# Performance work log

Measured on AMD Instinct MI355X. Metric: run time of the kernel, lower is better.

The kernel has to match this reference:

```python
import jax, jax.numpy as jnp
import numpy as np

GROUPS = 32
EPS = 1e-5

def group_norm(x, scale, bias):
    b, c, h, w = x.shape
    xg = x.reshape(b, GROUPS, c // GROUPS, h, w)
    mean = xg.mean(axis=(2, 3, 4), keepdims=True)
    var = xg.var(axis=(2, 3, 4), keepdims=True)
    xg = (xg - mean) * jax.lax.rsqrt(var + EPS)
    x = xg.reshape(b, c, h, w)
    return x * scale[None, :, None, None] + bias[None, :, None, None]

def conv2d(x, w, b, pad):
    y = jax.lax.conv_general_dilated(
        x, w, window_strides=(1, 1), padding=[(pad, pad), (pad, pad)],
        dimension_numbers=('NCHW', 'OIHW', 'NCHW'))
    return y + b[None, :, None, None]

def setup_inputs() -> dict:
    key = jax.random.key(0)
    ks = jax.random.split(key, 16)
    B, Cin, Cout, H, W, TDIM, NCON = 4, 128, 128, 64, 64, 512, 4
    s = 0.05
    return {
        'x': jax.random.normal(ks[0], (B, Cin, H, W), jnp.float32),
        't': jax.random.normal(ks[1], (B, TDIM), jnp.float32),
        'aim': jax.random.randint(ks[2], (B,), 0, NCON),
        'cond': jax.random.normal(ks[3], (B, Cin, H, W), jnp.float32),
        'gn1_scale': jnp.ones((Cin,), jnp.float32),
        'gn1_bias': jnp.zeros((Cin,), jnp.float32),
        'conv1_w': jax.random.normal(ks[4], (Cout, Cin, 3, 3), jnp.float32) * s,
        'conv1_b': jnp.zeros((Cout,), jnp.float32),
        'mlp_w': jax.random.normal(ks[5], (Cout, TDIM), jnp.float32) * s,
        'mlp_b': jnp.zeros((Cout,), jnp.float32),
        'cond_w': jax.random.normal(ks[6], (Cout, Cin, 1, 1), jnp.float32) * s,
        'cond_b': jnp.zeros((Cout,), jnp.float32),
        'gn2_scale': jnp.ones((Cout,), jnp.float32),
        'gn2_bias': jnp.zeros((Cout,), jnp.float32),
        'conv2_w': jax.random.normal(ks[7], (Cout, Cout, 3, 3), jnp.float32) * s,
        'conv2_b': jnp.zeros((Cout,), jnp.float32),
        'contrast_embed': jax.random.normal(ks[8], (NCON, Cout, 1, 1), jnp.float32),
    }

def reference(x, t, aim, cond, gn1_scale, gn1_bias, conv1_w, conv1_b,
              mlp_w, mlp_b, cond_w, cond_b, gn2_scale, gn2_bias,
              conv2_w, conv2_b, contrast_embed):
    # block1: GN -> SiLU -> 3x3 conv
    h = conv2d(jax.nn.silu(group_norm(x, gn1_scale, gn1_bias)), conv1_w, conv1_b, 1)
    # time embedding: SiLU -> Linear, broadcast over spatial
    temb = jax.nn.silu(t) @ mlp_w.T + mlp_b  # (b, out_ch)
    h = h + temb[:, :, None, None]
    # spatial cross-attention with cond
    c = conv2d(cond, cond_w, cond_b, 0)  # 1x1 projection, (b, C, u, v)
    C = h.shape[1]
    score = jnp.einsum('bchw,bcuv->bhwuv', h, c)  # (b, h, w, u, v)
    # NOTE: softmax over dim=1 (the spatial h axis), as in the source
    score = jax.nn.softmax(score / jnp.sqrt(jnp.float32(C)), axis=1)
    h = h + jnp.einsum('bhwuv,bcuv->bchw', score, c)
    # contrast embedding lookup
    h = h + contrast_embed[aim]  # (b, C, 1, 1) broadcast
    # block2: GN -> SiLU -> (dropout=identity at eval) -> 3x3 conv
    h = conv2d(jax.nn.silu(group_norm(h, gn2_scale, gn2_bias)), conv2_w, conv2_b, 1)
    # res_conv is Identity since in_ch == out_ch
    return h + x
```

## Files before the change

### kernel.cpp

```cpp
#include <hip/hip_runtime.h>
#include <cmath>

#define BB 4
#define CC 128
#define HH 64
#define WW 64
#define SP 4096
#define NG 32
#define TT 64
#define NS 2
#define PSZ ((size_t)BB * SP * CC)

typedef __bf16 bf16x8 __attribute__((ext_vector_type(8)));
typedef __bf16 bf16x4 __attribute__((ext_vector_type(4)));
typedef float  f32x4  __attribute__((ext_vector_type(4)));

__device__ __forceinline__ float silu_f(float v) {
    return v / (1.f + __expf(-v));
}

__global__ __launch_bounds__(256) void prep_kernel(
    const float* __restrict__ x, const float* __restrict__ gn1s,
    const float* __restrict__ gn1b, __bf16* __restrict__ aT,
    const float* __restrict__ c1w, const float* __restrict__ c2w,
    __bf16* __restrict__ wt,
    const float* __restrict__ t, const float* __restrict__ mlpw,
    const float* __restrict__ mlpb, float* __restrict__ tembw,
    const float* __restrict__ cond, const float* __restrict__ cw,
    const float* __restrict__ cb, __bf16* __restrict__ cmT,
    __bf16* __restrict__ cm2)
{
    __shared__ __align__(16) char pool[18432];
    __shared__ float rs[4], rs2[4], mean_s, inv_s;
    const int blk = blockIdx.x;
    const int tid = threadIdx.x;

    if (blk < 128) {
        const int b = blk >> 5, g = blk & 31;
        const float* p = x + (size_t)blk * 16384;
        float s = 0.f, s2 = 0.f;
        for (int it = 0; it < 16; ++it) {
            int q = it * 256 + tid;
            float4 v = *(const float4*)&p[q * 4];
            s += v.x + v.y + v.z + v.w;
            s2 += v.x * v.x + v.y * v.y + v.z * v.z + v.w * v.w;
        }
        #pragma unroll
        for (int off = 32; off >= 1; off >>= 1) {
            s  += __shfl_down(s,  off, 64);
            s2 += __shfl_down(s2, off, 64);
        }
        const int wid = tid >> 6;
        if ((tid & 63) == 0) { rs[wid] = s; rs2[wid] = s2; }
        __syncthreads();
        if (tid == 0) {
            float S = rs[0] + rs[1] + rs[2] + rs[3];
            float S2 = rs2[0] + rs2[1] + rs2[2] + rs2[3];
            float m = S * (1.f / 16384.f);
            float var = S2 * (1.f / 16384.f) - m * m;
            mean_s = m;
            inv_s = rsqrtf(var + 1e-5f);
        }
        __syncthreads();
        const float m = mean_s, inv = inv_s;
        float sc[4], bi[4];
        #pragma unroll
        for (int j = 0; j < 4; ++j) { sc[j] = gn1s[g * 4 + j]; bi[j] = gn1b[g * 4 + j]; }
        for (int it = 0; it < 16; ++it) {
            int pp = it * 256 + tid;
            bf16x4 o;
            #pragma unroll
            for (int j = 0; j < 4; ++j)
                o[j] = (__bf16)silu_f((p[j * 4096 + pp] - m) * inv * sc[j] + bi[j]);
            *(bf16x4*)&aT[((size_t)(b * SP + pp)) * CC + g * 4] = o;
        }
    } else if (blk < 146) {
        const int idx = blk - 128;
        const int wsel = idx / 9, tap = idx % 9;
        const float* src = wsel ? c2w : c1w;
        __bf16* dst = wt + (size_t)wsel * 9 * 16384 + (size_t)tap * 16384;
        for (int it = 0; it < 64; ++it) {
            int q = it * 256 + tid;
            dst[q] = (__bf16)src[(size_t)q * 9 + tap];
        }
    } else if (blk < 154) {
        const int cog = blk - 146;
        float* st = (float*)pool;
        for (int it = 0; it < 8; ++it) {
            int q = it * 256 + tid;
            st[q] = silu_f(t[q]);
        }
        __syncthreads();
        const int col = tid >> 4, seg = tid & 15;
        const float* wr = mlpw + (size_t)(cog * 16 + col) * 512 + seg * 32;
        float acc[4] = {0.f, 0.f, 0.f, 0.f};
        #pragma unroll
        for (int k8 = 0; k8 < 8; ++k8) {
            float4 wv = *(const float4*)&wr[k8 * 4];
            #pragma unroll
            for (int j = 0; j < 4; ++j) {
                int k = seg * 32 + k8 * 4 + j;
                float w4 = (&wv.x)[j];
                acc[0] += st[0 * 512 + k] * w4;
                acc[1] += st[1 * 512 + k] * w4;
                acc[2] += st[2 * 512 + k] * w4;
                acc[3] += st[3 * 512 + k] * w4;
            }
        }
        #pragma unroll
        for (int o = 1; o < 16; o <<= 1) {
            #pragma unroll
            for (int b4 = 0; b4 < 4; ++b4)
                acc[b4] += __shfl_xor(acc[b4], o, 64);
        }
        if (seg == 0) {
            float bv = mlpb[cog * 16 + col];
            #pragma unroll
            for (int b4 = 0; b4 < 4; ++b4)
                tembw[b4 * 128 + cog * 16 + col] = acc[b4] + bv;
        }
    } else {
        const int pblk = blk - 154;
        const int b = pblk >> 6;
        const int p0 = (pblk & 63) * 64;
        const int l = tid & 63, wv = tid >> 6;
        const int l15 = l & 15, l4 = l >> 4;
        const int mB = wv * 32;

        __bf16* XT = (__bf16*)pool;

        for (int it = 0; it < 32; ++it) {
            int q = it * 256 + tid;
            float v = cond[((size_t)(b * CC + (q >> 6))) * SP + p0 + (q & 63)];
            XT[(q & 63) * 136 + (q >> 6)] = (__bf16)v;
        }
        __syncthreads();

        f32x4 acc[2][4];
        #pragma unroll
        for (int mb = 0; mb < 2; ++mb)
            #pragma unroll
            for (int nt = 0; nt < 4; ++nt) acc[mb][nt] = (f32x4){0.f, 0.f, 0.f, 0.f};

        #pragma unroll
        for (int ks = 0; ks < 4; ++ks) {
            bf16x8 bfr[4];
            #pragma unroll
            for (int nt = 0; nt < 4; ++nt)
                bfr[nt] = *(const bf16x8*)&XT[(nt * 16 + l15) * 136 + ks * 32 + l4 * 8];
            #pragma unroll
            for (int mb = 0; mb < 2; ++mb) {
                const float* wrow = cw + (size_t)(mB + mb * 16 + l15) * 128 + ks * 32 + l4 * 8;
                float4 wa = *(const float4*)wrow;
                float4 wb4 = *(const float4*)(wrow + 4);
                bf16x8 afr;
                afr[0] = (__bf16)wa.x; afr[1] = (__bf16)wa.y;
                afr[2] = (__bf16)wa.z; afr[3] = (__bf16)wa.w;
                afr[4] = (__bf16)wb4.x; afr[5] = (__bf16)wb4.y;
                afr[6] = (__bf16)wb4.z; afr[7] = (__bf16)wb4.w;
                #pragma unroll
                for (int nt = 0; nt < 4; ++nt)
                    acc[mb][nt] = __builtin_amdgcn_mfma_f32_16x16x32_bf16(afr, bfr[nt], acc[mb][nt], 0, 0, 0);
            }
        }

        const float scl = 0.088388347648318447f;
        #pragma unroll
        for (int mb = 0; mb < 2; ++mb) {
            int co0 = mB + mb * 16 + l4 * 4;
            float bv[4];
            #pragma unroll
            for (int r = 0; r < 4; ++r) bv[r] = cb[co0 + r];
            #pragma unroll
            for (int nt = 0; nt < 4; ++nt) {
                int p = p0 + nt * 16 + l15;
                bf16x4 o;
                #pragma unroll
                for (int r = 0; r < 4; ++r)
                    o[r] = (__bf16)((acc[mb][nt][r] + bv[r]) * scl);
                *(bf16x4*)&cmT[((size_t)(b * SP + p)) * CC + co0] = o;
            }
        }
        __syncthreads();
        __bf16* O2 = (__bf16*)pool;
        #pragma unroll
        for (int mb = 0; mb < 2; ++mb) {
            int co0 = mB + mb * 16 + l4 * 4;
            #pragma unroll
            for (int r = 0; r < 4; ++r) {
                float bv = cb[co0 + r];
                #pragma unroll
                for (int nt = 0; nt < 4; ++nt)
                    O2[(co0 + r) * 72 + nt * 16 + l15] = (__bf16)(acc[mb][nt][r] + bv);
            }
        }
        __syncthreads();
        #pragma unroll
        for (int it = 0; it < 4; ++it) {
            int q = it * 256 + tid;
            int co = q >> 3, pc = q & 7;
            *(bf16x8*)&cm2[((size_t)(b * CC + co)) * SP + p0 + pc * 8] =
                *(const bf16x8*)&O2[co * 72 + pc * 8];
        }
    }
}

template<bool FUSE_TEMB, bool OUT_CF>
__global__ __launch_bounds__(256, 4) void conv_mfma_kernel(
    const __bf16* __restrict__ inT, const __bf16* __restrict__ wt,
    const float* __restrict__ bias, const float* __restrict__ temb,
    const float* __restrict__ resid, __bf16* __restrict__ outT,
    float* __restrict__ outF)
{
    const int y   = blockIdx.x >> 2;
    const int xh2 = (blockIdx.x >> 1) & 1;
    const int coh = blockIdx.x & 1;
    const int x0  = xh2 * 32;
    const int b   = blockIdx.y;
    const int tid = threadIdx.x;
    const int l = tid & 63, wv = tid >> 6;
    const int l15 = l & 15, l4 = l >> 4;
    const int co_w = coh * 64 + wv * 16;

    __shared__ __bf16 inS[3 * 16 * 34 * 8];

    const __bf16* inTb = inT + (size_t)b * SP * CC;
    for (int q = tid; q < 3 * 34 * 16; q += 256) {
        int cc = q & 15;
        int t2 = q >> 4;
        int xs = t2 % 34;
        int r  = t2 / 34;
        int yy = y + r - 1;
        int xg = x0 + xs - 1;
        bf16x8 v;
        if (((unsigned)yy < 64u) && ((unsigned)xg < 64u)) {
            v = *(const bf16x8*)&inTb[((size_t)(yy * 64 + xg)) * CC + cc * 8];
        } else {
            #pragma unroll
            for (int j = 0; j < 8; ++j) v[j] = (__bf16)0.f;
        }
        *(bf16x8*)&inS[((r * 16 + cc) * 34 + xs) * 8] = v;
    }
    __syncthreads();

    f32x4 acc[2];
    acc[0] = (f32x4){0.f, 0.f, 0.f, 0.f};
    acc[1] = (f32x4){0.f, 0.f, 0.f, 0.f};

    const __bf16* wp = wt + (size_t)(co_w + l15) * 128 + l4 * 8;
    bf16x8 wb[2][4];
    #pragma unroll
    for (int ks = 0; ks < 4; ++ks)
        wb[0][ks] = *(const bf16x8*)(wp + ks * 32);

    #pragma unroll
    for (int tap = 0; tap < 9; ++tap) {
        const int cur = tap & 1, nxt = cur ^ 1;
        if (tap < 8) {
            #pragma unroll
            for (int ks = 0; ks < 4; ++ks)
                wb[nxt][ks] = *(const bf16x8*)(wp + (tap + 1) * 16384 + ks * 32);
        }
        const int rr = tap / 3, dx = tap % 3;
        #pragma unroll
        for (int ks = 0; ks < 4; ++ks) {
            const __bf16* rb = &inS[((rr * 16 + ks * 4 + l4) * 34) * 8];
            bf16x8 b0 = *(const bf16x8*)&rb[(dx + l15) * 8];
            bf16x8 b1 = *(const bf16x8*)&rb[(16 + dx + l15) * 8];
            acc[0] = __builtin_amdgcn_mfma_f32_16x16x32_bf16(wb[cur][ks], b0, acc[0], 0, 0, 0);
            acc[1] = __builtin_amdgcn_mfma_f32_16x16x32_bf16(wb[cur][ks], b1, acc[1], 0, 0, 0);
        }
    }

    if (OUT_CF) {
        #pragma unroll
        for (int r = 0; r < 4; ++r) {
            int co = co_w + l4 * 4 + r;
            float bv = bias[co];
            #pragma unroll
            for (int nb = 0; nb < 2; ++nb) {
                int p = y * 64 + x0 + nb * 16 + l15;
                size_t o = ((size_t)(b * CC + co)) * SP + p;
                outF[o] = acc[nb][r] + bv + resid[o];
            }
        }
    } else {
        int co0 = co_w + l4 * 4;
        float bv[4];
        #pragma unroll
        for (int r = 0; r < 4; ++r)
            bv[r] = bias[co0 + r] + (FUSE_TEMB ? temb[b * CC + co0 + r] : 0.f);
        #pragma unroll
        for (int nb = 0; nb < 2; ++nb) {
            int p = y * 64 + x0 + nb * 16 + l15;
            bf16x4 o;
            #pragma unroll
            for (int r = 0; r < 4; ++r)
                o[r] = (__bf16)(acc[nb][r] + bv[r]);
            *(bf16x4*)&outT[((size_t)(b * SP + p)) * CC + co0] = o;
        }
    }
}

#define CT2 72
#define PBS 72
#define POOL_BYTES 46080

__global__ __launch_bounds__(256, 3) void attn_kernel(
    const __bf16* __restrict__ h1T, const __bf16* __restrict__ cmT,
    const __bf16* __restrict__ cm2, __bf16* __restrict__ parts)
{
    const int w = blockIdx.x;
    const int b = blockIdx.y;
    const int s = blockIdx.z;
    const int tid = threadIdx.x;
    const int wl = tid >> 6;
    const int l = tid & 63, l15 = l & 15, l4 = l >> 4;
    const int hB = (wl & 1) * 32;
    const int cB = (wl >> 1) * 64;

    __shared__ __align__(16) char pool[POOL_BYTES];
    __bf16* ct2p = (__bf16*)pool;
    __bf16* Pb   = (__bf16*)(pool + 36864);
    __bf16* Otr  = (__bf16*)pool;

    const __bf16* h1Tb = h1T + (size_t)b * SP * CC;
    const __bf16* cmTb = cmT + (size_t)b * SP * CC;
    const __bf16* cm2b = cm2 + (size_t)b * CC * SP;

    bf16x8 hfr[4][4];
    #pragma unroll
    for (int nt = 0; nt < 4; ++nt)
        #pragma unroll
        for (int ks = 0; ks < 4; ++ks)
            hfr[nt][ks] = *(const bf16x8*)&h1Tb[((size_t)((nt * 16 + l15) * WW + w)) * CC + ks * 32 + l4 * 8];

    f32x4 acc2[2][4];
    #pragma unroll
    for (int mb = 0; mb < 2; ++mb)
        #pragma unroll
        for (int nt = 0; nt < 4; ++nt) acc2[mb][nt] = (f32x4){0.f, 0.f, 0.f, 0.f};

    const int sc = tid >> 3;
    const int stc = tid & 7;

    {
        const int uv0 = s * TT;
        #pragma unroll
        for (int it = 0; it < 4; ++it) {
            int c = it * 32 + sc;
            *(bf16x8*)&ct2p[c * CT2 + stc * 8] =
                *(const bf16x8*)&cm2b[(size_t)c * SP + uv0 + stc * 8];
        }
        const __bf16* arow = cmTb + (size_t)(uv0 + 16 * wl + l15) * CC;
        bf16x8 afr[4];
        #pragma unroll
        for (int ks = 0; ks < 4; ++ks) afr[ks] = *(const bf16x8*)&arow[ks * 32 + l4 * 8];
        f32x4 s1[4];
        #pragma unroll
        for (int nt = 0; nt < 4; ++nt) {
            s1[nt] = (f32x4){0.f, 0.f, 0.f, 0.f};
            #pragma unroll
            for (int ks = 0; ks < 4; ++ks)
                s1[nt] = __builtin_amdgcn_mfma_f32_16x16x32_bf16(afr[ks], hfr[nt][ks], s1[nt], 0, 0, 0);
        }
        #pragma unroll
        for (int r = 0; r < 4; ++r) {
            float e0 = __expf(s1[0][r]), e1 = __expf(s1[1][r]);
            float e2 = __expf(s1[2][r]), e3 = __expf(s1[3][r]);
            float sm = e0 + e1 + e2 + e3;
            sm += __shfl_xor(sm, 1, 64);
            sm += __shfl_xor(sm, 2, 64);
            sm += __shfl_xor(sm, 4, 64);
            sm += __shfl_xor(sm, 8, 64);
            float ri = 1.f / sm;
            s1[0][r] = e0 * ri; s1[1][r] = e1 * ri;
            s1[2][r] = e2 * ri; s1[3][r] = e3 * ri;
        }
        #pragma unroll
        for (int nt = 0; nt < 4; ++nt) {
            bf16x4 pk;
            pk[0] = (__bf16)s1[nt][0]; pk[1] = (__bf16)s1[nt][1];
            pk[2] = (__bf16)s1[nt][2]; pk[3] = (__bf16)s1[nt][3];
            *(bf16x4*)&Pb[(nt * 16 + l15) * PBS + 16 * wl + l4 * 4] = pk;
        }
    }

    for (int i = 0; i < SP / TT / NS; ++i) {
        const int cur = i & 1;
        __syncthreads();
        bf16x8 st4[4];
        bf16x8 afr[4];
        if (i < SP / TT / NS - 1) {
            const int uv0n = ((i + 1) * NS + s) * TT;
            #pragma unroll
            for (int it = 0; it < 4; ++it) {
                int c = it * 32 + sc;
                st4[it] = *(const bf16x8*)&cm2b[(size_t)c * SP + uv0n + stc * 8];
            }
            const __bf16* arow = cmTb + (size_t)(uv0n + 16 * wl + l15) * CC;
            #pragma unroll
            for (int ks = 0; ks < 4; ++ks) afr[ks] = *(const bf16x8*)&arow[ks * 32 + l4 * 8];
        }
        bf16x8 pfr[2][2];
        #pragma unroll
        for (int mb = 0; mb < 2; ++mb)
            #pragma unroll
            for (int ks = 0; ks < 2; ++ks)
                pfr[mb][ks] = *(const bf16x8*)&Pb[(hB + mb * 16 + l15) * PBS + ks * 32 + l4 * 8];
        __syncthreads();
        {
            const __bf16* ctR = ct2p + cur * 9216;
            #pragma unroll
            for (int mb = 0; mb < 2; ++mb)
                #pragma unroll
                for (int nt = 0; nt < 4; ++nt)
                    #pragma unroll
                    for (int ks = 0; ks < 2; ++ks) {
                        bf16x8 bfr = *(const bf16x8*)&ctR[(cB + nt * 16 + l15) * CT2 + ks * 32 + l4 * 8];
                        acc2[mb][nt] = __builtin_amdgcn_mfma_f32_16x16x32_bf16(
                            pfr[mb][ks], bfr, acc2[mb][nt], 0, 0, 0);
                    }
        }
        if (i < SP / TT / NS - 1) {
            __bf16* ctW = ct2p + (cur ^ 1) * 9216;
            #pragma unroll
            for (int it = 0; it < 4; ++it) {
                int c = it * 32 + sc;
                *(bf16x8*)&ctW[c * CT2 + stc * 8] = st4[it];
            }
            f32x4 s1[4];
            #pragma unroll
            for (int nt = 0; nt < 4; ++nt) {
                s1[nt] = (f32x4){0.f, 0.f, 0.f, 0.f};
                #pragma unroll
                for (int ks = 0; ks < 4; ++ks)
                    s1[nt] = __builtin_amdgcn_mfma_f32_16x16x32_bf16(afr[ks], hfr[nt][ks], s1[nt], 0, 0, 0);
            }
            #pragma unroll
            for (int r = 0; r < 4; ++r) {
                float e0 = __expf(s1[0][r]), e1 = __expf(s1[1][r]);
                float e2 = __expf(s1[2][r]), e3 = __expf(s1[3][r]);
                float sm = e0 + e1 + e2 + e3;
                sm += __shfl_xor(sm, 1, 64);
                sm += __shfl_xor(sm, 2, 64);
                sm += __shfl_xor(sm, 4, 64);
                sm += __shfl_xor(sm, 8, 64);
                float ri = 1.f / sm;
                s1[0][r] = e0 * ri; s1[1][r] = e1 * ri;
                s1[2][r] = e2 * ri; s1[3][r] = e3 * ri;
            }
            #pragma unroll
            for (int nt = 0; nt < 4; ++nt) {
                bf16x4 pk;
                pk[0] = (__bf16)s1[nt][0]; pk[1] = (__bf16)s1[nt][1];
                pk[2] = (__bf16)s1[nt][2]; pk[3] = (__bf16)s1[nt][3];
                *(bf16x4*)&Pb[(nt * 16 + l15) * PBS + 16 * wl + l4 * 4] = pk;
            }
        }
    }

    __syncthreads();
    #pragma unroll
    for (int mb = 0; mb < 2; ++mb)
        #pragma unroll
        for (int nt = 0; nt < 4; ++nt)
            #pragma unroll
            for (int r = 0; r < 4; ++r)
                Otr[(hB + mb * 16 + l4 * 4 + r) * 136 + cB + nt * 16 + l15] =
                    (__bf16)acc2[mb][nt][r];
    __syncthreads();
    __bf16* pO = parts + (size_t)s * PSZ;
    #pragma unroll
    for (int it = 0; it < 4; ++it) {
        int q = it * 256 + tid;
        int h = q >> 4, cc = q & 15;
        *(bf16x8*)&pO[((size_t)(b * SP + h * WW + w)) * CC + cc * 8] =
            *(const bf16x8*)&Otr[h * 136 + cc * 8];
    }
}

__global__ __launch_bounds__(256) void gn2_stats_kernel(
    const __bf16* __restrict__ h1T, const __bf16* __restrict__ parts,
    const int* __restrict__ aim, const float* __restrict__ emb,
    __bf16* __restrict__ h2T, float* __restrict__ pstat)
{
    const int pb = blockIdx.x, b = blockIdx.y;
    const int tid = threadIdx.x;
    const int c4 = tid & 31;
    const float4 ev = *(const float4*)&emb[aim[b] * CC + c4 * 4];
    float s = 0.f, s2 = 0.f;
    for (int it = 0; it < 8; ++it) {
        int prow = it * 8 + (tid >> 5);
        size_t base = ((size_t)(b * SP + pb * 64 + prow)) * CC + c4 * 4;
        bf16x4 hv = *(const bf16x4*)&h1T[base];
        float v0 = (float)hv[0] + ev.x;
        float v1 = (float)hv[1] + ev.y;
        float v2 = (float)hv[2] + ev.z;
        float v3 = (float)hv[3] + ev.w;
        #pragma unroll
        for (int k = 0; k < NS; ++k) {
            bf16x4 a = *(const bf16x4*)&parts[(size_t)k * PSZ + base];
            v0 += (float)a[0]; v1 += (float)a[1];
            v2 += (float)a[2]; v3 += (float)a[3];
        }
        bf16x4 o;
        o[0] = (__bf16)v0; o[1] = (__bf16)v1;
        o[2] = (__bf16)v2; o[3] = (__bf16)v3;
        *(bf16x4*)&h2T[base] = o;
        s += v0 + v1 + v2 + v3;
        s2 += v0 * v0 + v1 * v1 + v2 * v2 + v3 * v3;
    }
    s  += __shfl_down(s,  32, 64);
    s2 += __shfl_down(s2, 32, 64);
    __shared__ float ls[4][32][2];
    const int wv = tid >> 6, ll = tid & 63;
    if (ll < 32) { ls[wv][ll][0] = s; ls[wv][ll][1] = s2; }
    __syncthreads();
    if (tid < 32) {
        float S = ls[0][tid][0] + ls[1][tid][0] + ls[2][tid][0] + ls[3][tid][0];
        float S2 = ls[0][tid][1] + ls[1][tid][1] + ls[2][tid][1] + ls[3][tid][1];
        int g = tid;
        pstat[(((size_t)b * NG + g) * 64 + pb) * 2]     = S;
        pstat[(((size_t)b * NG + g) * 64 + pb) * 2 + 1] = S2;
    }
}

__global__ __launch_bounds__(256) void gn2_apply_kernel(
    const __bf16* __restrict__ h2T, const float* __restrict__ pstat,
    const float* __restrict__ scale, const float* __restrict__ bias,
    __bf16* __restrict__ outT)
{
    const int pb = blockIdx.x, b = blockIdx.y;
    const int tid = threadIdx.x;
    const int c4 = tid & 31;
    const int g = c4;
    __shared__ float st[32][2];
    if (tid < 32) {
        float S = 0.f, S2 = 0.f;
        const float* ps = pstat + ((size_t)b * NG + tid) * 128;
        for (int k = 0; k < 64; ++k) { S += ps[k * 2]; S2 += ps[k * 2 + 1]; }
        float mm = S * (1.f / 16384.f);
        float var = S2 * (1.f / 16384.f) - mm * mm;
        st[tid][0] = mm;
        st[tid][1] = rsqrtf(var + 1e-5f);
    }
    __syncthreads();
    const float4 sc = *(const float4*)&scale[c4 * 4];
    const float4 bi = *(const float4*)&bias[c4 * 4];
    const float m = st[g][0], inv = st[g][1];
    for (int it = 0; it < 8; ++it) {
        int prow = it * 8 + (tid >> 5);
        size_t base = ((size_t)(b * SP + pb * 64 + prow)) * CC + c4 * 4;
        bf16x4 hv = *(const bf16x4*)&h2T[base];
        bf16x4 o;
        o[0] = (__bf16)silu_f(((float)hv[0] - m) * inv * sc.x + bi.x);
        o[1] = (__bf16)silu_f(((float)hv[1] - m) * inv * sc.y + bi.y);
        o[2] = (__bf16)silu_f(((float)hv[2] - m) * inv * sc.z + bi.z);
        o[3] = (__bf16)silu_f(((float)hv[3] - m) * inv * sc.w + bi.w);
        *(bf16x4*)&outT[base] = o;
    }
}

extern "C" void kernel_launch(void* const* d_in, const int* in_sizes, int n_in,
                              void* d_out, int out_size, void* d_ws, size_t ws_size,
                              hipStream_t stream)
{
    const float* x     = (const float*)d_in[0];
    const float* t     = (const float*)d_in[1];
    const int*   aim   = (const int*)  d_in[2];
    const float* cond  = (const float*)d_in[3];
    const float* gn1s  = (const float*)d_in[4];
    const float* gn1b  = (const float*)d_in[5];
    const float* c1w   = (const float*)d_in[6];
    const float* c1b   = (const float*)d_in[7];
    const float* mlpw  = (const float*)d_in[8];
    const float* mlpb  = (const float*)d_in[9];
    const float* cw    = (const float*)d_in[10];
    const float* cb    = (const float*)d_in[11];
    const float* gn2s  = (const float*)d_in[12];
    const float* gn2b  = (const float*)d_in[13];
    const float* c2w   = (const float*)d_in[14];
    const float* c2b   = (const float*)d_in[15];
    const float* emb   = (const float*)d_in[16];
    float* out = (float*)d_out;
    float* ws = (float*)d_ws;

    __bf16* aT    = (__bf16*)ws;
    __bf16* h1T   = (__bf16*)(ws + 1048576);
    __bf16* cmT   = (__bf16*)(ws + 2097152);
    __bf16* cm2   = (__bf16*)(ws + 3145728);
    __bf16* parts = (__bf16*)(ws + 4194304);
    __bf16* wt    = (__bf16*)(ws + 6291456);
    float*  tembw = ws + 6438912;
    float*  pstat = ws + 6439424;
    __bf16* h2T   = cmT;

    prep_kernel<<<dim3(410), dim3(256), 0, stream>>>(
        x, gn1s, gn1b, aT, c1w, c2w, wt, t, mlpw, mlpb, tembw,
        cond, cw, cb, cmT, cm2);
    conv_mfma_kernel<true, false><<<dim3(256, BB), dim3(256), 0, stream>>>(
        aT, wt, c1b, tembw, nullptr, h1T, nullptr);
    attn_kernel<<<dim3(WW, BB, NS), dim3(256), 0, stream>>>(h1T, cmT, cm2, parts);
    gn2_stats_kernel<<<dim3(64, BB), dim3(256), 0, stream>>>(h1T, parts, aim, emb, h2T, pstat);
    gn2_apply_kernel<<<dim3(64, BB), dim3(256), 0, stream>>>(h2T, pstat, gn2s, gn2b, aT);
    conv_mfma_kernel<false, true><<<dim3(256, BB), dim3(256), 0, stream>>>(
        aT, wt + (size_t)9 * 16384, c2b, nullptr, x, nullptr, out);
}
```

Measured before the change: 229.8 us.

## Fuse GN2 apply into conv2 load, atomic stats, double-buffer attention P tile

Drops the separate gn2_apply kernel. The second conv now reads the raw h2T and applies the group-norm affine plus SiLU while staging its input tile into shared memory. GN2 statistics are accumulated with atomicAdd into a small zeroed buffer instead of per-block partials that had to be re-reduced, which adds a memset launch. Separately, the attention kernel double-buffers its softmax P tile in LDS to remove one barrier per iteration, at the cost of more shared memory and lower occupancy (launch bound 3 to 2).

```diff
diff --git a/kernel.cpp b/kernel.cpp
--- a/kernel.cpp
+++ b/kernel.cpp
@@ -205,12 +205,13 @@
     }
 }
 
-template<bool FUSE_TEMB, bool OUT_CF>
+template<bool FUSE_TEMB, bool OUT_CF, bool FUSE_GN>
 __global__ __launch_bounds__(256, 4) void conv_mfma_kernel(
     const __bf16* __restrict__ inT, const __bf16* __restrict__ wt,
     const float* __restrict__ bias, const float* __restrict__ temb,
     const float* __restrict__ resid, __bf16* __restrict__ outT,
-    float* __restrict__ outF)
+    float* __restrict__ outF, const float* __restrict__ gstat,
+    const float* __restrict__ gn_s, const float* __restrict__ gn_b)
 {
     const int y   = blockIdx.x >> 2;
     const int xh2 = (blockIdx.x >> 1) & 1;
@@ -223,6 +224,21 @@
     const int co_w = coh * 64 + wv * 16;
 
     __shared__ __bf16 inS[3 * 16 * 34 * 8];
+    __shared__ float af[128], bfp[128];
+
+    if (FUSE_GN) {
+        if (tid < 128) {
+            int g = tid >> 2;
+            float S = gstat[(b * NG + g) * 2], S2 = gstat[(b * NG + g) * 2 + 1];
+            float m = S * (1.f / 16384.f);
+            float var = S2 * (1.f / 16384.f) - m * m;
+            float inv = rsqrtf(var + 1e-5f);
+            float a = inv * gn_s[tid];
+            af[tid] = a;
+            bfp[tid] = gn_b[tid] - m * a;
+        }
+        __syncthreads();
+    }
 
     const __bf16* inTb = inT + (size_t)b * SP * CC;
     for (int q = tid; q < 3 * 34 * 16; q += 256) {
@@ -234,7 +250,16 @@
         int xg = x0 + xs - 1;
         bf16x8 v;
         if (((unsigned)yy < 64u) && ((unsigned)xg < 64u)) {
-            v = *(const bf16x8*)&inTb[((size_t)(yy * 64 + xg)) * CC + cc * 8];
+            bf16x8 raw = *(const bf16x8*)&inTb[((size_t)(yy * 64 + xg)) * CC + cc * 8];
+            if (FUSE_GN) {
+                #pragma unroll
+                for (int j = 0; j < 8; ++j) {
+                    int c = cc * 8 + j;
+                    v[j] = (__bf16)silu_f((float)raw[j] * af[c] + bfp[c]);
+                }
+            } else {
+                v = raw;
+            }
         } else {
             #pragma unroll
             for (int j = 0; j < 8; ++j) v[j] = (__bf16)0.f;
@@ -304,9 +329,9 @@
 
 #define CT2 72
 #define PBS 72
-#define POOL_BYTES 46080
-
-__global__ __launch_bounds__(256, 3) void attn_kernel(
+#define POOL_BYTES 55296
+
+__global__ __launch_bounds__(256, 2) void attn_kernel(
     const __bf16* __restrict__ h1T, const __bf16* __restrict__ cmT,
     const __bf16* __restrict__ cm2, __bf16* __restrict__ parts)
 {
@@ -321,7 +346,7 @@
 
     __shared__ __align__(16) char pool[POOL_BYTES];
     __bf16* ct2p = (__bf16*)pool;
-    __bf16* Pb   = (__bf16*)(pool + 36864);
+    __bf16* Pbp  = (__bf16*)(pool + 36864);
     __bf16* Otr  = (__bf16*)pool;
 
     const __bf16* h1Tb = h1T + (size_t)b * SP * CC;
@@ -382,7 +407,7 @@
             bf16x4 pk;
             pk[0] = (__bf16)s1[nt][0]; pk[1] = (__bf16)s1[nt][1];
             pk[2] = (__bf16)s1[nt][2]; pk[3] = (__bf16)s1[nt][3];
-            *(bf16x4*)&Pb[(nt * 16 + l15) * PBS + 16 * wl + l4 * 4] = pk;
+            *(bf16x4*)&Pbp[(nt * 16 + l15) * PBS + 16 * wl + l4 * 4] = pk;
         }
     }
 
@@ -402,15 +427,15 @@
             #pragma unroll
             for (int ks = 0; ks < 4; ++ks) afr[ks] = *(const bf16x8*)&arow[ks * 32 + l4 * 8];
         }
-        bf16x8 pfr[2][2];
-        #pragma unroll
-        for (int mb = 0; mb < 2; ++mb)
-            #pragma unroll
-            for (int ks = 0; ks < 2; ++ks)
-                pfr[mb][ks] = *(const bf16x8*)&Pb[(hB + mb * 16 + l15) * PBS + ks * 32 + l4 * 8];
-        __syncthreads();
         {
+            const __bf16* PbR = Pbp + cur * 4608;
             const __bf16* ctR = ct2p + cur * 9216;
+            bf16x8 pfr[2][2];
+            #pragma unroll
+            for (int mb = 0; mb < 2; ++mb)
+                #pragma unroll
+                for (int ks = 0; ks < 2; ++ks)
+                    pfr[mb][ks] = *(const bf16x8*)&PbR[(hB + mb * 16 + l15) * PBS + ks * 32 + l4 * 8];
             #pragma unroll
             for (int mb = 0; mb < 2; ++mb)
                 #pragma unroll
@@ -450,12 +475,13 @@
                 s1[0][r] = e0 * ri; s1[1][r] = e1 * ri;
                 s1[2][r] = e2 * ri; s1[3][r] = e3 * ri;
             }
+            __bf16* PbW = Pbp + (cur ^ 1) * 4608;
             #pragma unroll
             for (int nt = 0; nt < 4; ++nt) {
                 bf16x4 pk;
                 pk[0] = (__bf16)s1[nt][0]; pk[1] = (__bf16)s1[nt][1];
                 pk[2] = (__bf16)s1[nt][2]; pk[3] = (__bf16)s1[nt][3];
-                *(bf16x4*)&Pb[(nt * 16 + l15) * PBS + 16 * wl + l4 * 4] = pk;
+                *(bf16x4*)&PbW[(nt * 16 + l15) * PBS + 16 * wl + l4 * 4] = pk;
             }
         }
     }
@@ -483,7 +509,7 @@
 __global__ __launch_bounds__(256) void gn2_stats_kernel(
     const __bf16* __restrict__ h1T, const __bf16* __restrict__ parts,
     const int* __restrict__ aim, const float* __restrict__ emb,
-    __bf16* __restrict__ h2T, float* __restrict__ pstat)
+    __bf16* __restrict__ h2T, float* __restrict__ gstat)
 {
     const int pb = blockIdx.x, b = blockIdx.y;
     const int tid = threadIdx.x;
@@ -520,45 +546,8 @@
     if (tid < 32) {
         float S = ls[0][tid][0] + ls[1][tid][0] + ls[2][tid][0] + ls[3][tid][0];
         float S2 = ls[0][tid][1] + ls[1][tid][1] + ls[2][tid][1] + ls[3][tid][1];
-        int g = tid;
-        pstat[(((size_t)b * NG + g) * 64 + pb) * 2]     = S;
-        pstat[(((size_t)b * NG + g) * 64 + pb) * 2 + 1] = S2;
-    }
-}
-
-__global__ __launch_bounds__(256) void gn2_apply_kernel(
-    const __bf16* __restrict__ h2T, const float* __restrict__ pstat,
-    const float* __restrict__ scale, const float* __restrict__ bias,
-    __bf16* __restrict__ outT)
-{
-    const int pb = blockIdx.x, b = blockIdx.y;
-    const int tid = threadIdx.x;
-    const int c4 = tid & 31;
-    const int g = c4;
-    __shared__ float st[32][2];
-    if (tid < 32) {
-        float S = 0.f, S2 = 0.f;
-        const float* ps = pstat + ((size_t)b * NG + tid) * 128;
-        for (int k = 0; k < 64; ++k) { S += ps[k * 2]; S2 += ps[k * 2 + 1]; }
-        float mm = S * (1.f / 16384.f);
-        float var = S2 * (1.f / 16384.f) - mm * mm;
-        st[tid][0] = mm;
-        st[tid][1] = rsqrtf(var + 1e-5f);
-    }
-    __syncthreads();
-    const float4 sc = *(const float4*)&scale[c4 * 4];
-    const float4 bi = *(const float4*)&bias[c4 * 4];
-    const float m = st[g][0], inv = st[g][1];
-    for (int it = 0; it < 8; ++it) {
-        int prow = it * 8 + (tid >> 5);
-        size_t base = ((size_t)(b * SP + pb * 64 + prow)) * CC + c4 * 4;
-        bf16x4 hv = *(const bf16x4*)&h2T[base];
-        bf16x4 o;
-        o[0] = (__bf16)silu_f(((float)hv[0] - m) * inv * sc.x + bi.x);
-        o[1] = (__bf16)silu_f(((float)hv[1] - m) * inv * sc.y + bi.y);
-        o[2] = (__bf16)silu_f(((float)hv[2] - m) * inv * sc.z + bi.z);
-        o[3] = (__bf16)silu_f(((float)hv[3] - m) * inv * sc.w + bi.w);
-        *(bf16x4*)&outT[base] = o;
+        atomicAdd(&gstat[(b * NG + tid) * 2], S);
+        atomicAdd(&gstat[(b * NG + tid) * 2 + 1], S2);
     }
 }
 
@@ -593,17 +582,17 @@
     __bf16* parts = (__bf16*)(ws + 4194304);
     __bf16* wt    = (__bf16*)(ws + 6291456);
     float*  tembw = ws + 6438912;
-    float*  pstat = ws + 6439424;
+    float*  gstat = ws + 6439424;
     __bf16* h2T   = cmT;
 
     prep_kernel<<<dim3(410), dim3(256), 0, stream>>>(
         x, gn1s, gn1b, aT, c1w, c2w, wt, t, mlpw, mlpb, tembw,
         cond, cw, cb, cmT, cm2);
-    conv_mfma_kernel<true, false><<<dim3(256, BB), dim3(256), 0, stream>>>(
-        aT, wt, c1b, tembw, nullptr, h1T, nullptr);
+    hipMemsetAsync(gstat, 0, 256 * sizeof(float), stream);
+    conv_mfma_kernel<true, false, false><<<dim3(256, BB), dim3(256), 0, stream>>>(
+        aT, wt, c1b, tembw, nullptr, h1T, nullptr, nullptr, nullptr, nullptr);
     attn_kernel<<<dim3(WW, BB, NS), dim3(256), 0, stream>>>(h1T, cmT, cm2, parts);
-    gn2_stats_kernel<<<dim3(64, BB), dim3(256), 0, stream>>>(h1T, parts, aim, emb, h2T, pstat);
-    gn2_apply_kernel<<<dim3(64, BB), dim3(256), 0, stream>>>(h2T, pstat, gn2s, gn2b, aT);
-    conv_mfma_kernel<false, true><<<dim3(256, BB), dim3(256), 0, stream>>>(
-        aT, wt + (size_t)9 * 16384, c2b, nullptr, x, nullptr, out);
+    gn2_stats_kernel<<<dim3(64, BB), dim3(256), 0, stream>>>(h1T, parts, aim, emb, h2T, gstat);
+    conv_mfma_kernel<false, true, true><<<dim3(256, BB), dim3(256), 0, stream>>>(
+        h2T, wt + (size_t)9 * 16384, c2b, nullptr, x, nullptr, out, gstat, gn2s, gn2b);
 }
```

After: 225.5 us. Within noise of the previous version (-1.9%).
